# Kernel tuning notes

Measured on AMD Instinct MI355X. Metric: run time of the kernel, lower is better.

Reference implementation:

```python
import jax, jax.numpy as jnp
import numpy as np

SIZE = 11
SIGMA = 1.5
PAD = 5

def _window2d():
    # cv2.getGaussianKernel(11, 1.5): normalized 1D Gaussian, outer product -> 2D window
    x = np.arange(SIZE) - (SIZE - 1) / 2.0
    g = np.exp(-(x * x) / (2.0 * SIGMA * SIGMA))
    g = g / g.sum()
    return jnp.asarray(np.outer(g, g), dtype=jnp.float32)

def _gconv(x, w):
    # x: [H, W]; replicate ('edge') pad by 5 then valid 11x11 correlation (matches torch
    # Conv2d with padding_mode='replicate'); output [H, W]
    xp = jnp.pad(x, PAD, mode='edge')[None, None]  # [1,1,H+10,W+10]
    y = jax.lax.conv_general_dilated(
        xp, w[None, None], window_strides=(1, 1), padding='VALID',
        dimension_numbers=('NCHW', 'OIHW', 'NCHW'))
    return y[0, 0]

def setup_inputs() -> dict:
    key = jax.random.key(0)
    k1, k2 = jax.random.split(key)
    H = W = 4096
    img1 = jax.random.uniform(k1, (H, W), dtype=jnp.float32) * 255.0
    img2 = jax.random.uniform(k2, (H, W), dtype=jnp.float32) * 255.0
    return {"img1": img1, "img2": img2}

def reference(img1, img2):
    w = _window2d()
    C1 = (0.01 * 255) ** 2
    C2 = (0.03 * 255) ** 2
    mu1 = _gconv(img1, w)
    mu2 = _gconv(img2, w)
    mu1_sq = mu1 * mu1
    mu2_sq = mu2 * mu2
    mu1_mu2 = mu1 * mu2
    sigma1_sq = _gconv(img1 * img1, w) - mu1_sq
    sigma2_sq = _gconv(img2 * img2, w) - mu2_sq
    sigma12 = _gconv(img1 * img2, w) - mu1_mu2
    ssim_map = (2 * mu1_mu2 + C1) * (2 * sigma12 + C2) / (
        (mu1_sq + mu2_sq + C1) * (sigma1_sq + sigma2_sq + C2))
    return jnp.mean(ssim_map)
```

## Files before the change

kernel.cpp:

```cpp
#include <hip/hip_runtime.h>
#include <cmath>

#define IMG_H 4096
#define IMG_W 4096
#define GX 32
#define GY 64
#define TCOLS 128
#define WCOLS 64
#define R 64
#define NITER (R + 10)
#define SW 80
#define RWORDS (2*SW)
#define NBUF 3
#define NWV 2

struct GW { float w[11]; };

__device__ __forceinline__ int clampi(int v, int lo, int hi) {
  return v < lo ? lo : (v > hi ? hi : v);
}

__global__ __launch_bounds__(128, 4) void ssim_sweep_kernel(
    const float* __restrict__ img1, const float* __restrict__ img2,
    float* __restrict__ partial, GW gw) {
  __shared__ __align__(16) float sbuf[NWV][NBUF][RWORDS];

  const int tid  = threadIdx.x;
  const int wv   = tid >> 6;
  const int lane = tid & 63;
  const int bx = blockIdx.x, by = blockIdx.y;
  const int cw   = bx * TCOLS + wv * WCOLS;
  const int row0 = by * R;
  const bool ledge = (cw == 0), redge = (cw + WCOLS == IMG_W);

  const float* srcp = (lane < 20) ? img1 : img2;
  const int    co   = clampi(cw - 8 + 4 * ((lane < 20) ? lane : lane - 20),
                             0, IMG_W - 4);

  float* swv = &sbuf[wv][0][0];

  auto stage = [&](int slot, int i) {
    const int gr = clampi(row0 - 5 + i, 0, IMG_H - 1);
    const long rb = (long)gr * IMG_W;
    float* dst = swv + slot * RWORDS;
    if (lane < 40) {
      __builtin_amdgcn_global_load_lds(
          (const __attribute__((address_space(1))) void*)(srcp + rb + co),
          (__attribute__((address_space(3))) void*)dst, 16, 0, 0);
    }
  };

  stage(0, 0);
  stage(1, 1);

  float A[4][11];
  float sum = 0.f;
  const float C1 = 6.5025f, C2 = 58.5225f;
  const int wl = lane + 3;

  int cur = 0;

  #pragma unroll 1
  for (int i = 0; i < NITER; ++i) {
    const int pre = (cur == 0) ? 2 : cur - 1;
    stage(pre, i + 2);

    asm volatile("s_waitcnt vmcnt(2)" ::: "memory");
    __builtin_amdgcn_sched_barrier(0);

    float* buf = swv + cur * RWORDS;
    cur = (cur == 2) ? 0 : cur + 1;

    if (ledge || redge) {
      if (lane < 16) {
        const int im = lane >> 3, l = lane & 7;
        const int srcw = im * SW + (ledge ? 8 : 71);
        const int dstw = im * SW + (ledge ? l : 72 + l);
        buf[dstw] = buf[srcw];
      }
    }

    float h0 = 0.f, h1 = 0.f, h2 = 0.f, h3 = 0.f;
    #pragma unroll
    for (int j = 0; j <= 10; ++j) {
      const float a = buf[wl + j];
      const float b = buf[SW + wl + j];
      const float w = gw.w[j];
      const float sq = fmaf(b, b, a * a);
      const float ab = a * b;
      h0 = fmaf(w, a,  h0);
      h1 = fmaf(w, b,  h1);
      h2 = fmaf(w, sq, h2);
      h3 = fmaf(w, ab, h3);
    }

    #pragma unroll
    for (int k = 0; k < 10; ++k) {
      A[0][k] = fmaf(gw.w[10 - k], h0, A[0][k + 1]);
      A[1][k] = fmaf(gw.w[10 - k], h1, A[1][k + 1]);
      A[2][k] = fmaf(gw.w[10 - k], h2, A[2][k + 1]);
      A[3][k] = fmaf(gw.w[10 - k], h3, A[3][k + 1]);
    }
    A[0][10] = gw.w[0] * h0;
    A[1][10] = gw.w[0] * h1;
    A[2][10] = gw.w[0] * h2;
    A[3][10] = gw.w[0] * h3;

    if (i >= 10) {
      const float mu1 = A[0][0], mu2 = A[1][0];
      const float s3  = A[2][0], s4  = A[3][0];
      const float mu1s = mu1 * mu1, mu2s = mu2 * mu2, m12 = mu1 * mu2;
      const float num = (2.f * m12 + C1) * (2.f * (s4 - m12) + C2);
      const float den = (mu1s + mu2s + C1) * ((s3 - mu1s - mu2s) + C2);
      sum += num * __builtin_amdgcn_rcpf(den);
    }
  }

  #pragma unroll
  for (int off = 32; off > 0; off >>= 1) sum += __shfl_down(sum, off);
  __shared__ float wsum[NWV];
  if (lane == 0) wsum[wv] = sum;
  __syncthreads();
  if (tid == 0)
    partial[by * GX + bx] = wsum[0] + wsum[1];
}

__global__ __launch_bounds__(256) void ssim_reduce_kernel(
    const float* __restrict__ partial, float* __restrict__ out) {
  int tid = threadIdx.x;
  double s = 0.0;
  #pragma unroll
  for (int k = 0; k < 8; ++k) s += (double)partial[tid + 256 * k];
  #pragma unroll
  for (int off = 32; off > 0; off >>= 1) s += __shfl_down(s, off);
  __shared__ double ws[4];
  if ((tid & 63) == 0) ws[tid >> 6] = s;
  __syncthreads();
  if (tid == 0)
    out[0] = (float)((ws[0] + ws[1] + ws[2] + ws[3]) /
                     ((double)IMG_H * (double)IMG_W));
}

extern "C" void kernel_launch(void* const* d_in, const int* in_sizes, int n_in,
                              void* d_out, int out_size, void* d_ws, size_t ws_size,
                              hipStream_t stream) {
  const float* img1 = (const float*)d_in[0];
  const float* img2 = (const float*)d_in[1];
  float* partial = (float*)d_ws;
  float* out = (float*)d_out;

  GW gw;
  double g[11], s = 0.0;
  for (int i = 0; i < 11; ++i) {
    double x = i - 5.0;
    g[i] = exp(-(x * x) / (2.0 * 1.5 * 1.5));
    s += g[i];
  }
  for (int i = 0; i < 11; ++i) gw.w[i] = (float)(g[i] / s);

  dim3 grid(GX, GY);
  ssim_sweep_kernel<<<grid, 128, 0, stream>>>(img1, img2, partial, gw);
  ssim_reduce_kernel<<<1, 256, 0, stream>>>(partial, out);
}
```

Measured before the change: 185.7 us.

## Process two rows per sweep iteration with four-slot LDS ring

Unrolls the row sweep by two: each iteration stages two new rows into a four-slot LDS ring, computes two horizontal convolutions together and updates the vertical shift register for two rows at once. This halves loop overhead and the per-row wait/barrier cost and exposes more independent ILP between the two rows. In exchange it uses more registers and LDS, and the occupancy hint is lowered from 4 to 3 blocks per CU. NITER is even (74), so the paired loop covers all rows.

```diff
diff --git a/kernel.cpp b/kernel.cpp
--- a/kernel.cpp
+++ b/kernel.cpp
@@ -9,9 +9,10 @@
 #define WCOLS 64
 #define R 64
 #define NITER (R + 10)
+#define NDIT (NITER / 2)
 #define SW 80
 #define RWORDS (2*SW)
-#define NBUF 3
+#define NBUF 4
 #define NWV 2
 
 struct GW { float w[11]; };
@@ -20,7 +21,7 @@
   return v < lo ? lo : (v > hi ? hi : v);
 }
 
-__global__ __launch_bounds__(128, 4) void ssim_sweep_kernel(
+__global__ __launch_bounds__(128, 3) void ssim_sweep_kernel(
     const float* __restrict__ img1, const float* __restrict__ img2,
     float* __restrict__ partial, GW gw) {
   __shared__ __align__(16) float sbuf[NWV][NBUF][RWORDS];
@@ -58,61 +59,89 @@
   const float C1 = 6.5025f, C2 = 58.5225f;
   const int wl = lane + 3;
 
-  int cur = 0;
+  #pragma unroll 1
+  for (int t = 0; t < NDIT; ++t) {
+    const int i = 2 * t;
+    const int s0 = i & 3, s1 = (i + 1) & 3, s2 = (i + 2) & 3, s3 = (i + 3) & 3;
 
-  #pragma unroll 1
-  for (int i = 0; i < NITER; ++i) {
-    const int pre = (cur == 0) ? 2 : cur - 1;
-    stage(pre, i + 2);
+    stage(s2, i + 2);
+    stage(s3, i + 3);
 
     asm volatile("s_waitcnt vmcnt(2)" ::: "memory");
     __builtin_amdgcn_sched_barrier(0);
 
-    float* buf = swv + cur * RWORDS;
-    cur = (cur == 2) ? 0 : cur + 1;
+    float* buf0 = swv + s0 * RWORDS;
+    float* buf1 = swv + s1 * RWORDS;
 
     if (ledge || redge) {
-      if (lane < 16) {
-        const int im = lane >> 3, l = lane & 7;
+      if (lane < 32) {
+        const int bsel = lane >> 4;
+        const int im   = (lane >> 3) & 1;
+        const int l    = lane & 7;
+        float* bp = bsel ? buf1 : buf0;
         const int srcw = im * SW + (ledge ? 8 : 71);
         const int dstw = im * SW + (ledge ? l : 72 + l);
-        buf[dstw] = buf[srcw];
+        bp[dstw] = bp[srcw];
       }
     }
 
-    float h0 = 0.f, h1 = 0.f, h2 = 0.f, h3 = 0.f;
+    float h00 = 0.f, h01 = 0.f, h02 = 0.f, h03 = 0.f;
+    float h10 = 0.f, h11 = 0.f, h12 = 0.f, h13 = 0.f;
     #pragma unroll
     for (int j = 0; j <= 10; ++j) {
-      const float a = buf[wl + j];
-      const float b = buf[SW + wl + j];
       const float w = gw.w[j];
-      const float sq = fmaf(b, b, a * a);
-      const float ab = a * b;
-      h0 = fmaf(w, a,  h0);
-      h1 = fmaf(w, b,  h1);
-      h2 = fmaf(w, sq, h2);
-      h3 = fmaf(w, ab, h3);
+      {
+        const float a = buf0[wl + j];
+        const float b = buf0[SW + wl + j];
+        const float sq = fmaf(b, b, a * a);
+        const float ab = a * b;
+        h00 = fmaf(w, a,  h00);
+        h01 = fmaf(w, b,  h01);
+        h02 = fmaf(w, sq, h02);
+        h03 = fmaf(w, ab, h03);
+      }
+      {
+        const float a = buf1[wl + j];
+        const float b = buf1[SW + wl + j];
+        const float sq = fmaf(b, b, a * a);
+        const float ab = a * b;
+        h10 = fmaf(w, a,  h10);
+        h11 = fmaf(w, b,  h11);
+        h12 = fmaf(w, sq, h12);
+        h13 = fmaf(w, ab, h13);
+      }
+    }
+    const float h0[4] = {h00, h01, h02, h03};
+    const float h1[4] = {h10, h11, h12, h13};
+
+    float o0[4], o1[4];
+    #pragma unroll
+    for (int ch = 0; ch < 4; ++ch) {
+      o0[ch] = fmaf(gw.w[10], h0[ch], A[ch][1]);
+      #pragma unroll
+      for (int k = 0; k < 9; ++k)
+        A[ch][k] = fmaf(gw.w[10 - k], h1[ch],
+                        fmaf(gw.w[9 - k], h0[ch], A[ch][k + 2]));
+      A[ch][9]  = fmaf(gw.w[1], h1[ch], gw.w[0] * h0[ch]);
+      A[ch][10] = gw.w[0] * h1[ch];
+      o1[ch] = A[ch][0];
     }
 
-    #pragma unroll
-    for (int k = 0; k < 10; ++k) {
-      A[0][k] = fmaf(gw.w[10 - k], h0, A[0][k + 1]);
-      A[1][k] = fmaf(gw.w[10 - k], h1, A[1][k + 1]);
-      A[2][k] = fmaf(gw.w[10 - k], h2, A[2][k + 1]);
-      A[3][k] = fmaf(gw.w[10 - k], h3, A[3][k + 1]);
-    }
-    A[0][10] = gw.w[0] * h0;
-    A[1][10] = gw.w[0] * h1;
-    A[2][10] = gw.w[0] * h2;
-    A[3][10] = gw.w[0] * h3;
-
     if (i >= 10) {
-      const float mu1 = A[0][0], mu2 = A[1][0];
-      const float s3  = A[2][0], s4  = A[3][0];
-      const float mu1s = mu1 * mu1, mu2s = mu2 * mu2, m12 = mu1 * mu2;
-      const float num = (2.f * m12 + C1) * (2.f * (s4 - m12) + C2);
-      const float den = (mu1s + mu2s + C1) * ((s3 - mu1s - mu2s) + C2);
-      sum += num * __builtin_amdgcn_rcpf(den);
+      {
+        const float mu1 = o0[0], mu2 = o0[1], s3v = o0[2], s4v = o0[3];
+        const float mu1s = mu1 * mu1, mu2s = mu2 * mu2, m12 = mu1 * mu2;
+        const float num = (2.f * m12 + C1) * (2.f * (s4v - m12) + C2);
+        const float den = (mu1s + mu2s + C1) * ((s3v - mu1s - mu2s) + C2);
+        sum += num * __builtin_amdgcn_rcpf(den);
+      }
+      {
+        const float mu1 = o1[0], mu2 = o1[1], s3v = o1[2], s4v = o1[3];
+        const float mu1s = mu1 * mu1, mu2s = mu2 * mu2, m12 = mu1 * mu2;
+        const float num = (2.f * m12 + C1) * (2.f * (s4v - m12) + C2);
+        const float den = (mu1s + mu2s + C1) * ((s3v - mu1s - mu2s) + C2);
+        sum += num * __builtin_amdgcn_rcpf(den);
+      }
     }
   }
 
```

Measured after the change: 180.9 us. 2.5% less time.

## Process four rows per iteration with an eight-slot prefetch ring and one-wave blocks

Applied to the files above, without the earlier changes.

The row sweep is unrolled by four. Each iteration prefetches four rows into an eight-slot LDS ring and waits with vmcnt(4), which deepens the load pipeline and amortises waits and loop overhead. The vertical accumulator is updated with four rows of horizontal sums at a time, and each output is finalised inline. Blocks become single 64-lane waves (grid doubled in x, no cross-wave reduction), which raises register pressure from the 4x4 partials and lowers the launch-bounds occupancy hint. The loop now covers 76 rows instead of 74, so it loads two extra clamped rows and guards outputs with a range check.

```diff
diff --git a/kernel.cpp b/kernel.cpp
--- a/kernel.cpp
+++ b/kernel.cpp
@@ -3,16 +3,15 @@
 
 #define IMG_H 4096
 #define IMG_W 4096
-#define GX 32
+#define GX 64
 #define GY 64
-#define TCOLS 128
 #define WCOLS 64
 #define R 64
 #define NITER (R + 10)
+#define NQIT 19
 #define SW 80
 #define RWORDS (2*SW)
-#define NBUF 3
-#define NWV 2
+#define NBUF 8
 
 struct GW { float w[11]; };
 
@@ -20,29 +19,25 @@
   return v < lo ? lo : (v > hi ? hi : v);
 }
 
-__global__ __launch_bounds__(128, 4) void ssim_sweep_kernel(
+__global__ __launch_bounds__(64, 3) void ssim_sweep_kernel(
     const float* __restrict__ img1, const float* __restrict__ img2,
     float* __restrict__ partial, GW gw) {
-  __shared__ __align__(16) float sbuf[NWV][NBUF][RWORDS];
+  __shared__ __align__(16) float sbuf[NBUF][RWORDS];
 
-  const int tid  = threadIdx.x;
-  const int wv   = tid >> 6;
-  const int lane = tid & 63;
+  const int lane = threadIdx.x;
   const int bx = blockIdx.x, by = blockIdx.y;
-  const int cw   = bx * TCOLS + wv * WCOLS;
+  const int cw   = bx * WCOLS;
   const int row0 = by * R;
-  const bool ledge = (cw == 0), redge = (cw + WCOLS == IMG_W);
+  const bool ledge = (bx == 0), redge = (bx == GX - 1);
 
   const float* srcp = (lane < 20) ? img1 : img2;
   const int    co   = clampi(cw - 8 + 4 * ((lane < 20) ? lane : lane - 20),
                              0, IMG_W - 4);
 
-  float* swv = &sbuf[wv][0][0];
-
   auto stage = [&](int slot, int i) {
     const int gr = clampi(row0 - 5 + i, 0, IMG_H - 1);
     const long rb = (long)gr * IMG_W;
-    float* dst = swv + slot * RWORDS;
+    float* dst = &sbuf[slot][0];
     if (lane < 40) {
       __builtin_amdgcn_global_load_lds(
           (const __attribute__((address_space(1))) void*)(srcp + rb + co),
@@ -50,79 +45,104 @@
     }
   };
 
-  stage(0, 0);
-  stage(1, 1);
+  stage(0, 0); stage(1, 1); stage(2, 2); stage(3, 3);
 
   float A[4][11];
   float sum = 0.f;
   const float C1 = 6.5025f, C2 = 58.5225f;
   const int wl = lane + 3;
 
-  int cur = 0;
+  #pragma unroll 1
+  for (int t = 0; t < NQIT; ++t) {
+    const int i = 4 * t;
 
-  #pragma unroll 1
-  for (int i = 0; i < NITER; ++i) {
-    const int pre = (cur == 0) ? 2 : cur - 1;
-    stage(pre, i + 2);
+    stage((i + 4) & 7, i + 4);
+    stage((i + 5) & 7, i + 5);
+    stage((i + 6) & 7, i + 6);
+    stage((i + 7) & 7, i + 7);
 
-    asm volatile("s_waitcnt vmcnt(2)" ::: "memory");
+    asm volatile("s_waitcnt vmcnt(4)" ::: "memory");
     __builtin_amdgcn_sched_barrier(0);
 
-    float* buf = swv + cur * RWORDS;
-    cur = (cur == 2) ? 0 : cur + 1;
+    float* buf0 = &sbuf[(i + 0) & 7][0];
+    float* buf1 = &sbuf[(i + 1) & 7][0];
+    float* buf2 = &sbuf[(i + 2) & 7][0];
+    float* buf3 = &sbuf[(i + 3) & 7][0];
 
     if (ledge || redge) {
-      if (lane < 16) {
-        const int im = lane >> 3, l = lane & 7;
-        const int srcw = im * SW + (ledge ? 8 : 71);
-        const int dstw = im * SW + (ledge ? l : 72 + l);
-        buf[dstw] = buf[srcw];
+      const int bsel = lane >> 4;
+      const int im   = (lane >> 3) & 1;
+      const int l    = lane & 7;
+      float* bp = &sbuf[(i + bsel) & 7][0];
+      const int srcw = im * SW + (ledge ? 8 : 71);
+      const int dstw = im * SW + (ledge ? l : 72 + l);
+      bp[dstw] = bp[srcw];
+    }
+
+    float h[4][4];
+    #pragma unroll
+    for (int r = 0; r < 4; ++r)
+      #pragma unroll
+      for (int ch = 0; ch < 4; ++ch) h[r][ch] = 0.f;
+    #pragma unroll
+    for (int j = 0; j <= 10; ++j) {
+      const float w = gw.w[j];
+      float* bufs[4] = {buf0, buf1, buf2, buf3};
+      #pragma unroll
+      for (int r = 0; r < 4; ++r) {
+        const float a = bufs[r][wl + j];
+        const float b = bufs[r][SW + wl + j];
+        const float sq = fmaf(b, b, a * a);
+        const float ab = a * b;
+        h[r][0] = fmaf(w, a,  h[r][0]);
+        h[r][1] = fmaf(w, b,  h[r][1]);
+        h[r][2] = fmaf(w, sq, h[r][2]);
+        h[r][3] = fmaf(w, ab, h[r][3]);
       }
     }
 
-    float h0 = 0.f, h1 = 0.f, h2 = 0.f, h3 = 0.f;
     #pragma unroll
-    for (int j = 0; j <= 10; ++j) {
-      const float a = buf[wl + j];
-      const float b = buf[SW + wl + j];
-      const float w = gw.w[j];
-      const float sq = fmaf(b, b, a * a);
-      const float ab = a * b;
-      h0 = fmaf(w, a,  h0);
-      h1 = fmaf(w, b,  h1);
-      h2 = fmaf(w, sq, h2);
-      h3 = fmaf(w, ab, h3);
+    for (int r = 0; r < 4; ++r) {
+      const int e = i - 10 + r;
+      if (e >= 0 && e < R) {
+        float o[4];
+        #pragma unroll
+        for (int ch = 0; ch < 4; ++ch) {
+          float v = A[ch][r + 1];
+          #pragma unroll
+          for (int q = 0; q <= r; ++q)
+            v = fmaf(gw.w[10 - r + q], h[q][ch], v);
+          o[ch] = v;
+        }
+        const float mu1 = o[0], mu2 = o[1], s3v = o[2], s4v = o[3];
+        const float mu1s = mu1 * mu1, mu2s = mu2 * mu2, m12 = mu1 * mu2;
+        const float num = (2.f * m12 + C1) * (2.f * (s4v - m12) + C2);
+        const float den = (mu1s + mu2s + C1) * ((s3v - mu1s - mu2s) + C2);
+        sum += num * __builtin_amdgcn_rcpf(den);
+      }
     }
 
     #pragma unroll
-    for (int k = 0; k < 10; ++k) {
-      A[0][k] = fmaf(gw.w[10 - k], h0, A[0][k + 1]);
-      A[1][k] = fmaf(gw.w[10 - k], h1, A[1][k + 1]);
-      A[2][k] = fmaf(gw.w[10 - k], h2, A[2][k + 1]);
-      A[3][k] = fmaf(gw.w[10 - k], h3, A[3][k + 1]);
-    }
-    A[0][10] = gw.w[0] * h0;
-    A[1][10] = gw.w[0] * h1;
-    A[2][10] = gw.w[0] * h2;
-    A[3][10] = gw.w[0] * h3;
-
-    if (i >= 10) {
-      const float mu1 = A[0][0], mu2 = A[1][0];
-      const float s3  = A[2][0], s4  = A[3][0];
-      const float mu1s = mu1 * mu1, mu2s = mu2 * mu2, m12 = mu1 * mu2;
-      const float num = (2.f * m12 + C1) * (2.f * (s4 - m12) + C2);
-      const float den = (mu1s + mu2s + C1) * ((s3 - mu1s - mu2s) + C2);
-      sum += num * __builtin_amdgcn_rcpf(den);
+    for (int ch = 0; ch < 4; ++ch) {
+      #pragma unroll
+      for (int k = 0; k < 7; ++k)
+        A[ch][k] = fmaf(gw.w[10 - k], h[3][ch],
+                   fmaf(gw.w[9 - k],  h[2][ch],
+                   fmaf(gw.w[8 - k],  h[1][ch],
+                   fmaf(gw.w[7 - k],  h[0][ch], A[ch][k + 4]))));
+      A[ch][7]  = fmaf(gw.w[3], h[3][ch],
+                  fmaf(gw.w[2], h[2][ch],
+                  fmaf(gw.w[1], h[1][ch], gw.w[0] * h[0][ch])));
+      A[ch][8]  = fmaf(gw.w[2], h[3][ch],
+                  fmaf(gw.w[1], h[2][ch], gw.w[0] * h[1][ch]));
+      A[ch][9]  = fmaf(gw.w[1], h[3][ch], gw.w[0] * h[2][ch]);
+      A[ch][10] = gw.w[0] * h[3][ch];
     }
   }
 
   #pragma unroll
   for (int off = 32; off > 0; off >>= 1) sum += __shfl_down(sum, off);
-  __shared__ float wsum[NWV];
-  if (lane == 0) wsum[wv] = sum;
-  __syncthreads();
-  if (tid == 0)
-    partial[by * GX + bx] = wsum[0] + wsum[1];
+  if (lane == 0) partial[by * GX + bx] = sum;
 }
 
 __global__ __launch_bounds__(256) void ssim_reduce_kernel(
@@ -130,7 +150,7 @@
   int tid = threadIdx.x;
   double s = 0.0;
   #pragma unroll
-  for (int k = 0; k < 8; ++k) s += (double)partial[tid + 256 * k];
+  for (int k = 0; k < 16; ++k) s += (double)partial[tid + 256 * k];
   #pragma unroll
   for (int off = 32; off > 0; off >>= 1) s += __shfl_down(s, off);
   __shared__ double ws[4];
@@ -159,6 +179,6 @@
   for (int i = 0; i < 11; ++i) gw.w[i] = (float)(g[i] / s);
 
   dim3 grid(GX, GY);
-  ssim_sweep_kernel<<<grid, 128, 0, stream>>>(img1, img2, partial, gw);
+  ssim_sweep_kernel<<<grid, 64, 0, stream>>>(img1, img2, partial, gw);
   ssim_reduce_kernel<<<1, 256, 0, stream>>>(partial, out);
 }
```

After: 189.4 us. 2.0% more time.
